# Performance work log

Measured on AMD Instinct MI355X. Metric: run time of the kernel, lower is better.

The kernel has to match this reference:

```python
import jax, jax.numpy as jnp
import numpy as np

N_SRC = 500000   # rows in source layer value tensor
B = 500000       # rule neurons in this layer
W = 8            # weights per rule (shared across all neurons)
D = 16           # per-neuron value dimension


def setup_inputs() -> dict:
    key = jax.random.key(0)
    k1, k2, k3 = jax.random.split(key, 3)
    values = jax.random.normal(k1, (N_SRC, D), dtype=jnp.float32)
    weights = jax.random.normal(k2, (W, D), dtype=jnp.float32)
    indices = jax.random.randint(k3, (W, B), 0, N_SRC, dtype=jnp.int64)
    return {"values": values, "weights": weights, "indices": indices}


def reference(values, weights, indices):
    # Per-weight irregular gather: [W, B, D]
    gathered = values[indices]
    # Weighted apply (elementwise per-weight transform), broadcast-sum over
    # the weight axis, then tanh -- same math as stack+sum+tanh in torch.
    y = jnp.tanh(jnp.sum(gathered * weights[:, None, :], axis=0))  # [B, D]
    return y
```

## Files before the change

kernel.cpp:

```cpp
#include <hip/hip_runtime.h>

#define NB   500000
#define NW   8
#define ND   16

__device__ __forceinline__ float fast_tanh(float x) {
    float e = __expf(2.0f * x);
    return 1.0f - 2.0f * __builtin_amdgcn_rcpf(e + 1.0f);
}

__global__ __launch_bounds__(256) void wrl_kernel(
    const float* __restrict__ values,
    const float* __restrict__ weights,
    const int*   __restrict__ indices,
    float* __restrict__ out)
{
    const int tid = blockIdx.x * 256 + threadIdx.x;
    if (tid >= NB * 4) return;
    const int b  = tid >> 2;
    const int dq = tid & 3;

    float4 wreg[NW];
#pragma unroll
    for (int w = 0; w < NW; ++w)
        wreg[w] = *reinterpret_cast<const float4*>(weights + w * ND + dq * 4);

    int idx[NW];
#pragma unroll
    for (int w = 0; w < NW; ++w)
        idx[w] = indices[w * NB + b];

    float4 acc = make_float4(0.f, 0.f, 0.f, 0.f);
#pragma unroll
    for (int w = 0; w < NW; ++w) {
        const float4 v = *reinterpret_cast<const float4*>(
            values + (size_t)idx[w] * ND + dq * 4);
        acc.x += v.x * wreg[w].x;
        acc.y += v.y * wreg[w].y;
        acc.z += v.z * wreg[w].z;
        acc.w += v.w * wreg[w].w;
    }

    float4 o;
    o.x = fast_tanh(acc.x);
    o.y = fast_tanh(acc.y);
    o.z = fast_tanh(acc.z);
    o.w = fast_tanh(acc.w);
    *reinterpret_cast<float4*>(out + (size_t)b * ND + dq * 4) = o;
}

extern "C" void kernel_launch(void* const* d_in, const int* in_sizes, int n_in,
                              void* d_out, int out_size, void* d_ws, size_t ws_size,
                              hipStream_t stream) {
    const float* values  = (const float*)d_in[0];
    const float* weights = (const float*)d_in[1];
    const int*   indices = (const int*)d_in[2];
    float* out = (float*)d_out;

    const int total  = NB * 4;
    const int blocks = (total + 255) / 256;
    wrl_kernel<<<blocks, 256, 0, stream>>>(values, weights, indices, out);
}
```

Before: 150.0 us.

## Use persistent grid-stride loop with software-prefetched indices and nontemporal accesses

Replaces the one-thread-per-quad launch with a fixed 2048-block grid where each thread handles four strided work items. Each iteration prefetches the next item's eight indices while the current gathers are still outstanding, so index-load latency overlaps with value gathers. Index loads and output stores become nontemporal so the streaming data does not take cache space away from the gathered values. This adds register pressure and tail clamping logic, and the fixed grid ties the work split to NB.

```diff
diff --git a/kernel.cpp b/kernel.cpp
--- a/kernel.cpp
+++ b/kernel.cpp
@@ -1,52 +1,78 @@
 #include <hip/hip_runtime.h>
 
-#define NB   500000
-#define NW   8
-#define ND   16
+#define NB     500000
+#define NW     8
+#define ND     16
+#define NTOT   (NB * 4)
+#define BLK    256
+#define GRID   2048
+#define STRIDE (GRID * BLK)
+#define ITERS  4
+
+typedef float f32x4 __attribute__((ext_vector_type(4)));
 
 __device__ __forceinline__ float fast_tanh(float x) {
     float e = __expf(2.0f * x);
     return 1.0f - 2.0f * __builtin_amdgcn_rcpf(e + 1.0f);
 }
 
-__global__ __launch_bounds__(256) void wrl_kernel(
+__global__ __launch_bounds__(BLK) void wrl_kernel(
     const float* __restrict__ values,
     const float* __restrict__ weights,
     const int*   __restrict__ indices,
     float* __restrict__ out)
 {
-    const int tid = blockIdx.x * 256 + threadIdx.x;
-    if (tid >= NB * 4) return;
-    const int b  = tid >> 2;
-    const int dq = tid & 3;
+    const int tid0 = blockIdx.x * BLK + threadIdx.x;
+    const int dq   = tid0 & 3;
 
-    float4 wreg[NW];
+    f32x4 wreg[NW];
 #pragma unroll
     for (int w = 0; w < NW; ++w)
-        wreg[w] = *reinterpret_cast<const float4*>(weights + w * ND + dq * 4);
+        wreg[w] = *reinterpret_cast<const f32x4*>(weights + w * ND + dq * 4);
 
-    int idx[NW];
+    int tid = tid0;
+    int bC  = (tid < NTOT ? tid : NTOT - 1) >> 2;
+    int idxC[NW];
 #pragma unroll
     for (int w = 0; w < NW; ++w)
-        idx[w] = indices[w * NB + b];
+        idxC[w] = __builtin_nontemporal_load(&indices[(size_t)w * NB + bC]);
 
-    float4 acc = make_float4(0.f, 0.f, 0.f, 0.f);
 #pragma unroll
-    for (int w = 0; w < NW; ++w) {
-        const float4 v = *reinterpret_cast<const float4*>(
-            values + (size_t)idx[w] * ND + dq * 4);
-        acc.x += v.x * wreg[w].x;
-        acc.y += v.y * wreg[w].y;
-        acc.z += v.z * wreg[w].z;
-        acc.w += v.w * wreg[w].w;
+    for (int it = 0; it < ITERS; ++it) {
+        const bool act = (tid < NTOT);
+        const int  b   = bC;
+
+        f32x4 v[NW];
+#pragma unroll
+        for (int w = 0; w < NW; ++w)
+            v[w] = *reinterpret_cast<const f32x4*>(
+                values + (size_t)idxC[w] * ND + dq * 4);
+
+        const int tidN = tid + STRIDE;
+        if (it < ITERS - 1) {
+            const int bN = (tidN < NTOT ? tidN : NTOT - 1) >> 2;
+#pragma unroll
+            for (int w = 0; w < NW; ++w)
+                idxC[w] = __builtin_nontemporal_load(&indices[(size_t)w * NB + bN]);
+            bC = bN;
+        }
+
+        f32x4 acc = (f32x4)(0.f);
+#pragma unroll
+        for (int w = 0; w < NW; ++w) {
+            acc.x += v[w].x * wreg[w].x;  acc.y += v[w].y * wreg[w].y;
+            acc.z += v[w].z * wreg[w].z;  acc.w += v[w].w * wreg[w].w;
+        }
+
+        if (act) {
+            f32x4 o;
+            o.x = fast_tanh(acc.x); o.y = fast_tanh(acc.y);
+            o.z = fast_tanh(acc.z); o.w = fast_tanh(acc.w);
+            __builtin_nontemporal_store(
+                o, reinterpret_cast<f32x4*>(out + (size_t)b * ND + dq * 4));
+        }
+        tid = tidN;
     }
-
-    float4 o;
-    o.x = fast_tanh(acc.x);
-    o.y = fast_tanh(acc.y);
-    o.z = fast_tanh(acc.z);
-    o.w = fast_tanh(acc.w);
-    *reinterpret_cast<float4*>(out + (size_t)b * ND + dq * 4) = o;
 }
 
 extern "C" void kernel_launch(void* const* d_in, const int* in_sizes, int n_in,
@@ -57,7 +83,5 @@
     const int*   indices = (const int*)d_in[2];
     float* out = (float*)d_out;
 
-    const int total  = NB * 4;
-    const int blocks = (total + 255) / 256;
-    wrl_kernel<<<blocks, 256, 0, stream>>>(values, weights, indices, out);
+    wrl_kernel<<<GRID, BLK, 0, stream>>>(values, weights, indices, out);
 }
```

After: 152.3 us. Within noise of the previous version (+1.5%).
